# Performance work log

Measured on AMD Instinct MI355X. Metric: run time of the kernel, lower is better.

Reference implementation:

```python
import jax, jax.numpy as jnp
import numpy as np

C_IN = 128
C_INNER = 128


def setup_inputs() -> dict:
    key = jax.random.key(0)
    ks = jax.random.split(key, 9)
    b, c, h, w = 4, C_IN, 64, 64
    s = 1.0 / np.sqrt(c)
    x = jax.random.normal(ks[0], (b, c, h, w), dtype=jnp.float32)
    Wq = jax.random.normal(ks[1], (C_INNER, C_IN), dtype=jnp.float32) * s
    bq = jnp.zeros((C_INNER,), dtype=jnp.float32)
    Wk = jax.random.normal(ks[2], (C_INNER, C_IN), dtype=jnp.float32) * s
    bk = jnp.zeros((C_INNER,), dtype=jnp.float32)
    Wv = jax.random.normal(ks[3], (C_INNER, C_IN), dtype=jnp.float32) * s
    bv = jnp.zeros((C_INNER,), dtype=jnp.float32)
    Wo = jax.random.normal(ks[4], (C_IN, C_INNER), dtype=jnp.float32) * (1.0 / np.sqrt(C_INNER))
    bo = jnp.zeros((C_IN,), dtype=jnp.float32)
    return {"x": x, "Wq": Wq, "bq": bq, "Wk": Wk, "bk": bk,
            "Wv": Wv, "bv": bv, "Wo": Wo, "bo": bo}


def _conv1x1(x, W, bias):
    # x: (b,c,h,w), W: (o,c) -> (b,o,h,w)
    return jnp.einsum('oc,bchw->bohw', W, x) + bias[None, :, None, None]


def reference(x, Wq, bq, Wk, bk, Wv, bv, Wo, bo):
    b, c, h, w = x.shape
    ci = Wq.shape[0]
    n = h * w
    q = _conv1x1(x, Wq, bq).reshape(b, ci, n)          # (b, ci, n)
    k = _conv1x1(x, Wk, bk).reshape(b, ci, n)          # (b, ci, n)
    v = _conv1x1(x, Wv, bv).reshape(b, ci, n)          # (b, ci, n)
    # attn = softmax(q^T @ k) over keys
    attn = jnp.einsum('bci,bcj->bij', q, k)            # (b, n, n)
    attn = jax.nn.softmax(attn, axis=-1)
    out = jnp.einsum('bij,bcj->bci', attn, v)          # (b, ci, n)
    out = out.reshape(b, ci, h, w)
    out = _conv1x1(out, Wo, bo)
    return out + x
```

## Files before the change

### kernel.cpp

```cpp
#include <hip/hip_runtime.h>
#include <math.h>
#include <stdint.h>

#define CDIM 128
#define NTOT 4096

typedef _Float16 f16x8 __attribute__((ext_vector_type(8)));
typedef float floatx4 __attribute__((ext_vector_type(4)));

static __device__ __forceinline__ floatx4 mfma16(f16x8 a, f16x8 b, floatx4 c) {
    return __builtin_amdgcn_mfma_f32_16x16x32_f16(a, b, c, 0, 0, 0);
}
static __device__ __forceinline__ unsigned short f2h(float f) {
    _Float16 h = (_Float16)f;
    return __builtin_bit_cast(unsigned short, h);
}
static __device__ __forceinline__ float h2f(unsigned short u) {
    return (float)__builtin_bit_cast(_Float16, u);
}

#define SWZ(row, cc) ((((row) << 7)) + ((((cc) ^ ((row) & 15))) << 3))
#define SWZ8(row, cc) ((((row) << 6)) + ((((cc) ^ ((row) & 7))) << 3))

static __device__ __forceinline__ void gload_lds16(const void* g, void* l) {
    __builtin_amdgcn_global_load_lds(
        (const __attribute__((address_space(1))) void*)g,
        (__attribute__((address_space(3))) void*)l, 16, 0, 0);
}

__global__ __launch_bounds__(256) void qkv_proj_kernel(
    const float* __restrict__ x,
    const float* __restrict__ Wq, const float* __restrict__ bq,
    const float* __restrict__ Wk, const float* __restrict__ bk,
    const float* __restrict__ Wv, const float* __restrict__ bv,
    unsigned short* __restrict__ qo, unsigned short* __restrict__ ko,
    unsigned short* __restrict__ vo)
{
    __shared__ __align__(16) unsigned short Xs[64][136];
    __shared__ __align__(16) unsigned short Ws[64][136];

    const int t = threadIdx.x, b = blockIdx.y, n0 = blockIdx.x * 64;
    const int zo = blockIdx.z * 64;
    const int w = t >> 6, quad = (t >> 4) & 3, l15 = t & 15;

    {
        const int n = (t & 15) * 4;
        const int c = (t >> 4) * 8;
        float4 xr[8];
        #pragma unroll
        for (int j = 0; j < 8; ++j)
            xr[j] = *(const float4*)&x[((size_t)b * CDIM + c + j) * NTOT + n0 + n];
        #pragma unroll
        for (int k = 0; k < 4; ++k) {
            ushort4 ulo, uhi;
            ulo.x = f2h(((const float*)&xr[0])[k]);
            ulo.y = f2h(((const float*)&xr[1])[k]);
            ulo.z = f2h(((const float*)&xr[2])[k]);
            ulo.w = f2h(((const float*)&xr[3])[k]);
            uhi.x = f2h(((const float*)&xr[4])[k]);
            uhi.y = f2h(((const float*)&xr[5])[k]);
            uhi.z = f2h(((const float*)&xr[6])[k]);
            uhi.w = f2h(((const float*)&xr[7])[k]);
            *(ushort4*)&Xs[n + k][c]     = ulo;
            *(ushort4*)&Xs[n + k][c + 4] = uhi;
        }
    }

    f16x8 xf[4];
    for (int s = 0; s < 3; ++s) {
        const float* W    = (s == 0) ? Wq : (s == 1) ? Wk : Wv;
        const float* bias = (s == 0) ? bq : (s == 1) ? bk : bv;
        if (s) __syncthreads();
        {
            int o = t >> 2, ch = (t & 3) * 32;
            #pragma unroll
            for (int i = 0; i < 8; ++i) {
                float4 f4 = *(const float4*)&W[(size_t)(zo + o) * CDIM + ch + i * 4];
                ushort4 u = { f2h(f4.x), f2h(f4.y), f2h(f4.z), f2h(f4.w) };
                *(ushort4*)&Ws[o][ch + i * 4] = u;
            }
        }
        __syncthreads();
        if (s == 0) {
            #pragma unroll
            for (int f = 0; f < 4; ++f)
                xf[f] = *(const f16x8*)&Xs[w * 16 + l15][f * 32 + quad * 8];
        }

        if (s < 2) {
            unsigned short* dst = (s == 0) ? qo : ko;
            #pragma unroll
            for (int ot = 0; ot < 4; ++ot) {
                floatx4 acc = (floatx4){0.f, 0.f, 0.f, 0.f};
                #pragma unroll
                for (int f = 0; f < 4; ++f) {
                    f16x8 aW = *(const f16x8*)&Ws[ot * 16 + l15][f * 32 + quad * 8];
                    acc = mfma16(aW, xf[f], acc);
                }
                const int ob = zo + ot * 16 + quad * 4;
                ushort4 u;
                u.x = f2h(acc[0] + bias[ob + 0]);
                u.y = f2h(acc[1] + bias[ob + 1]);
                u.z = f2h(acc[2] + bias[ob + 2]);
                u.w = f2h(acc[3] + bias[ob + 3]);
                *(ushort4*)&dst[((size_t)b * NTOT + n0 + w * 16 + l15) * CDIM + ob] = u;
            }
        } else {
            #pragma unroll
            for (int ot = 0; ot < 4; ++ot) {
                floatx4 acc = (floatx4){0.f, 0.f, 0.f, 0.f};
                #pragma unroll
                for (int f = 0; f < 4; ++f) {
                    f16x8 bW = *(const f16x8*)&Ws[ot * 16 + l15][f * 32 + quad * 8];
                    acc = mfma16(xf[f], bW, acc);
                }
                const int o = zo + ot * 16 + l15;
                const float bv_ = bias[o];
                ushort4 u;
                u.x = f2h(acc[0] + bv_); u.y = f2h(acc[1] + bv_);
                u.z = f2h(acc[2] + bv_); u.w = f2h(acc[3] + bv_);
                *(ushort4*)&vo[((size_t)b * CDIM + o) * NTOT + n0 + w * 16 + quad * 4] = u;
            }
        }
    }
}

__global__ __launch_bounds__(256, 2) void attn_kernel(
    const unsigned short* __restrict__ qg,
    const unsigned short* __restrict__ kg,
    const unsigned short* __restrict__ vg,
    unsigned short* __restrict__ Op,
    float* __restrict__ Ms, float* __restrict__ Ls)
{
    __shared__ __align__(16) unsigned short Kb[2][64 * 128];
    __shared__ __align__(16) unsigned short Vb[2][128 * 64];

    const int t = threadIdx.x;
    const int w = t >> 6, quad = (t >> 4) & 3, l15 = t & 15;

    const int bid = blockIdx.x;
    const int swz = ((bid & 7) << 6) | (bid >> 3);
    const int gidx = swz >> 5;
    const int b = gidx & 3;
    const int z = gidx >> 2;
    const int i0 = (swz & 31) * 128;
    const int jbase = z * 1024;
    const size_t vbase = (size_t)b * CDIM * NTOT;

    f16x8 bQ[2][4];
    #pragma unroll
    for (int nt = 0; nt < 2; ++nt) {
        const size_t qrow = ((size_t)b * NTOT + i0 + w * 32 + nt * 16 + l15) * CDIM;
        #pragma unroll
        for (int f = 0; f < 4; ++f)
            bQ[nt][f] = *(const f16x8*)&qg[qrow + f * 32 + quad * 8];
    }

    auto stage = [&](unsigned short* Kd, unsigned short* Vd, int j0) {
        const size_t kbase = ((size_t)b * NTOT + j0) * CDIM;
        const size_t vrow0 = vbase + j0;
        #pragma unroll
        for (int r = 0; r < 4; ++r) {
            const int flat = r * 256 + t;
            const int ldsoff = (r * 256 + (t & ~63)) * 8;
            const int krow = flat >> 4, kcc = flat & 15;
            gload_lds16(&kg[kbase + (size_t)krow * CDIM + ((kcc ^ (krow & 15)) << 3)],
                        &Kd[ldsoff]);
            const int vrow = flat >> 3, vcc = flat & 7;
            gload_lds16(&vg[vrow0 + (size_t)vrow * NTOT + ((vcc ^ (vrow & 7)) << 3)],
                        &Vd[ldsoff]);
        }
    };

    floatx4 accO[2][8];
    #pragma unroll
    for (int nt = 0; nt < 2; ++nt)
        #pragma unroll
        for (int dt = 0; dt < 8; ++dt) accO[nt][dt] = (floatx4){0.f, 0.f, 0.f, 0.f};
    float m_run[2] = {-INFINITY, -INFINITY};
    float l_part[2] = {0.f, 0.f};

    stage(Kb[0], Vb[0], jbase);

    for (int iter = 0; iter < 16; ++iter) {
        const int cur = iter & 1;

        asm volatile("s_waitcnt vmcnt(0) lgkmcnt(0)" ::: "memory");
        __builtin_amdgcn_s_barrier();

        if (iter < 15) stage(Kb[cur ^ 1], Vb[cur ^ 1], jbase + (iter + 1) * 64);

        floatx4 accT[2][4];
        #pragma unroll
        for (int nt = 0; nt < 2; ++nt)
            #pragma unroll
            for (int jt = 0; jt < 4; ++jt) accT[nt][jt] = (floatx4){0.f, 0.f, 0.f, 0.f};
        #pragma unroll
        for (int jt = 0; jt < 4; ++jt)
            #pragma unroll
            for (int f = 0; f < 4; ++f) {
                f16x8 aK = *(const f16x8*)&Kb[cur][SWZ(jt * 16 + l15, f * 4 + quad)];
                accT[0][jt] = mfma16(aK, bQ[0][f], accT[0][jt]);
                accT[1][jt] = mfma16(aK, bQ[1][f], accT[1][jt]);
            }

        float m_new[2], alpha[2];
        ushort4 pu[2][4];
        #pragma unroll
        for (int nt = 0; nt < 2; ++nt) {
            float tm = accT[nt][0][0];
            #pragma unroll
            for (int jt = 0; jt < 4; ++jt)
                #pragma unroll
                for (int r = 0; r < 4; ++r) tm = fmaxf(tm, accT[nt][jt][r]);
            tm = fmaxf(tm, __shfl_xor(tm, 16));
            tm = fmaxf(tm, __shfl_xor(tm, 32));
            m_new[nt] = fmaxf(m_run[nt], tm);
            alpha[nt] = __expf(m_run[nt] - m_new[nt]);
            m_run[nt] = m_new[nt];
            float ps = 0.f;
            #pragma unroll
            for (int jt = 0; jt < 4; ++jt) {
                float p0 = __expf(accT[nt][jt][0] - m_new[nt]);
                float p1 = __expf(accT[nt][jt][1] - m_new[nt]);
                float p2 = __expf(accT[nt][jt][2] - m_new[nt]);
                float p3 = __expf(accT[nt][jt][3] - m_new[nt]);
                ps += (p0 + p1) + (p2 + p3);
                pu[nt][jt].x = f2h(p0); pu[nt][jt].y = f2h(p1);
                pu[nt][jt].z = f2h(p2); pu[nt][jt].w = f2h(p3);
            }
            l_part[nt] = l_part[nt] * alpha[nt] + ps;
            #pragma unroll
            for (int dt = 0; dt < 8; ++dt) {
                accO[nt][dt][0] *= alpha[nt]; accO[nt][dt][1] *= alpha[nt];
                accO[nt][dt][2] *= alpha[nt]; accO[nt][dt][3] *= alpha[nt];
            }
        }

        asm volatile("s_waitcnt lgkmcnt(0)" ::: "memory");
        __builtin_amdgcn_s_barrier();

        unsigned short* Pb = Kb[cur];
        #pragma unroll
        for (int nt = 0; nt < 2; ++nt) {
            const int prow = w * 32 + nt * 16 + l15;
            #pragma unroll
            for (int jt = 0; jt < 4; ++jt)
                *(ushort4*)&Pb[SWZ8(prow, 2 * jt + (quad >> 1)) + (quad & 1) * 4] =
                    pu[nt][jt];
        }

        f16x8 bP[2][2];
        #pragma unroll
        for (int nt = 0; nt < 2; ++nt) {
            const int prow = w * 32 + nt * 16 + l15;
            #pragma unroll
            for (int kb = 0; kb < 2; ++kb)
                bP[nt][kb] = *(const f16x8*)&Pb[SWZ8(prow, kb * 4 + quad)];
        }
        #pragma unroll
        for (int dt = 0; dt < 8; ++dt)
            #pragma unroll
            for (int kb = 0; kb < 2; ++kb) {
                f16x8 aV = *(const f16x8*)&Vb[cur][SWZ8(dt * 16 + l15, kb * 4 + quad)];
                accO[0][dt] = mfma16(aV, bP[0][kb], accO[0][dt]);
                accO[1][dt] = mfma16(aV, bP[1][kb], accO[1][dt]);
            }
    }

    #pragma unroll
    for (int nt = 0; nt < 2; ++nt) {
        float lf = l_part[nt];
        lf += __shfl_xor(lf, 16);
        lf += __shfl_xor(lf, 32);
        const float inv = 1.0f / lf;
        const size_t orow =
            (((size_t)z * 4 + b) * NTOT + i0 + w * 32 + nt * 16 + l15) * CDIM;
        #pragma unroll
        for (int dt = 0; dt < 8; ++dt) {
            ushort4 u;
            u.x = f2h(accO[nt][dt][0] * inv); u.y = f2h(accO[nt][dt][1] * inv);
            u.z = f2h(accO[nt][dt][2] * inv); u.w = f2h(accO[nt][dt][3] * inv);
            *(ushort4*)&Op[orow + dt * 16 + quad * 4] = u;
        }
        if (quad == 0) {
            const int idx = (z * 4 + b) * NTOT + i0 + w * 32 + nt * 16 + l15;
            Ms[idx] = m_run[nt];
            Ls[idx] = lf;
        }
    }
}

__global__ __launch_bounds__(256) void out_proj_kernel(
    const unsigned short* __restrict__ Op,
    const float* __restrict__ Ms, const float* __restrict__ Ls,
    const float* __restrict__ Wo, const float* __restrict__ bo,
    const float* __restrict__ x, float* __restrict__ out)
{
    __shared__ __align__(16) unsigned short As[64][136];
    __shared__ __align__(16) unsigned short Ws[64][136];

    const int t = threadIdx.x, b = blockIdx.y, n0 = blockIdx.x * 64;
    const int zo = blockIdx.z * 64;
    const int w = t >> 6, quad = (t >> 4) & 3, l15 = t & 15;

    const size_t PER = (size_t)NTOT * 4 * CDIM;

    #pragma unroll
    for (int r = 0; r < 4; ++r) {
        int flat = r * 256 + t;
        int row = flat >> 4, c16 = (flat & 15) * 8;
        const int bn = b * NTOT + n0 + row;
        float m0 = Ms[bn], m1 = Ms[bn + 16384], m2 = Ms[bn + 32768], m3 = Ms[bn + 49152];
        float M = fmaxf(fmaxf(m0, m1), fmaxf(m2, m3));
        float w0 = Ls[bn]         * __expf(m0 - M);
        float w1 = Ls[bn + 16384] * __expf(m1 - M);
        float w2 = Ls[bn + 32768] * __expf(m2 - M);
        float w3 = Ls[bn + 49152] * __expf(m3 - M);
        const float inv = 1.0f / (w0 + w1 + w2 + w3);
        w0 *= inv; w1 *= inv; w2 *= inv; w3 *= inv;

        const size_t base = (size_t)bn * CDIM + c16;
        uint4 a0 = *(const uint4*)&Op[base];
        uint4 a1 = *(const uint4*)&Op[PER + base];
        uint4 a2 = *(const uint4*)&Op[2 * PER + base];
        uint4 a3 = *(const uint4*)&Op[3 * PER + base];
        const unsigned short* p0 = (const unsigned short*)&a0;
        const unsigned short* p1 = (const unsigned short*)&a1;
        const unsigned short* p2 = (const unsigned short*)&a2;
        const unsigned short* p3 = (const unsigned short*)&a3;
        unsigned short mv[8];
        #pragma unroll
        for (int j = 0; j < 8; ++j)
            mv[j] = f2h(w0 * h2f(p0[j]) + w1 * h2f(p1[j]) +
                        w2 * h2f(p2[j]) + w3 * h2f(p3[j]));
        *(uint4*)&As[row][c16] = *(const uint4*)mv;
    }
    {
        int o = t >> 2, ch = (t & 3) * 32;
        #pragma unroll
        for (int i = 0; i < 8; ++i) {
            float4 f4 = *(const float4*)&Wo[(size_t)(zo + o) * CDIM + ch + i * 4];
            ushort4 u = { f2h(f4.x), f2h(f4.y), f2h(f4.z), f2h(f4.w) };
            *(ushort4*)&Ws[o][ch + i * 4] = u;
        }
    }
    __syncthreads();

    f16x8 bA[4];
    #pragma unroll
    for (int f = 0; f < 4; ++f)
        bA[f] = *(const f16x8*)&As[w * 16 + l15][f * 32 + quad * 8];

    #pragma unroll
    for (int ot = 0; ot < 4; ++ot) {
        floatx4 acc = (floatx4){0.f, 0.f, 0.f, 0.f};
        #pragma unroll
        for (int f = 0; f < 4; ++f) {
            f16x8 aW = *(const f16x8*)&Ws[ot * 16 + l15][f * 32 + quad * 8];
            acc = mfma16(aW, bA[f], acc);
        }
        const int ob = zo + ot * 16 + quad * 4;
        #pragma unroll
        for (int r = 0; r < 4; ++r) {
            size_t idx = ((size_t)b * CDIM + ob + r) * NTOT + n0 + w * 16 + l15;
            out[idx] = acc[r] + bo[ob + r] + x[idx];
        }
    }
}

extern "C" void kernel_launch(void* const* d_in, const int* in_sizes, int n_in,
                              void* d_out, int out_size, void* d_ws, size_t ws_size,
                              hipStream_t stream)
{
    const float* x  = (const float*)d_in[0];
    const float* Wq = (const float*)d_in[1];
    const float* bq = (const float*)d_in[2];
    const float* Wk = (const float*)d_in[3];
    const float* bk = (const float*)d_in[4];
    const float* Wv = (const float*)d_in[5];
    const float* bv = (const float*)d_in[6];
    const float* Wo = (const float*)d_in[7];
    const float* bo = (const float*)d_in[8];
    float* out = (float*)d_out;

    const size_t PER = (size_t)4 * CDIM * NTOT;
    unsigned short* q_ws  = (unsigned short*)d_ws;
    unsigned short* k_ws  = q_ws + PER;
    unsigned short* v_ws  = k_ws + PER;
    unsigned short* op_ws = v_ws + PER;
    float*          ms_ws = (float*)(op_ws + 4 * PER);
    float*          ls_ws = ms_ws + 4 * 16384;

    qkv_proj_kernel<<<dim3(64, 4, 2), dim3(256), 0, stream>>>(
        x, Wq, bq, Wk, bk, Wv, bv, q_ws, k_ws, v_ws);
    attn_kernel<<<dim3(512, 1, 1), dim3(256), 0, stream>>>(
        q_ws, k_ws, v_ws, op_ws, ms_ws, ls_ws);
    out_proj_kernel<<<dim3(64, 4, 2), dim3(256), 0, stream>>>(
        op_ws, ms_ws, ls_ws, Wo, bo, x, out);
}
```

Baseline: 144.3 us.

## Pre-convert weights to fp16, single-buffer V, lazy softmax rescale, raise occupancy

Adds a small kernel that converts all four weight matrices to fp16 once. The projection kernels then read weights directly from global memory instead of converting them into LDS per block, which drops an LDS buffer and several barriers. In the attention kernel, V becomes single-buffered and is loaded within the iteration that uses it, with a partial vmcnt wait, so LDS shrinks and launch bounds can target three blocks per SM. Online-softmax rescaling is skipped unless the running max rises by more than 8, which saves exp and multiply work. The risks are exposed V load latency, an extra kernel launch, and a small fp16 overflow risk from the stale max.

```diff
diff --git a/kernel.cpp b/kernel.cpp
--- a/kernel.cpp
+++ b/kernel.cpp
@@ -28,16 +28,27 @@
         (__attribute__((address_space(3))) void*)l, 16, 0, 0);
 }
 
+__global__ __launch_bounds__(256) void wcvt_kernel(
+    const float* __restrict__ Wq, const float* __restrict__ Wk,
+    const float* __restrict__ Wv, const float* __restrict__ Wo,
+    unsigned short* __restrict__ Wh)
+{
+    const float* src = (blockIdx.y == 0) ? Wq : (blockIdx.y == 1) ? Wk
+                     : (blockIdx.y == 2) ? Wv : Wo;
+    const int i = (blockIdx.x * 256 + threadIdx.x) * 4;
+    float4 f = *(const float4*)&src[i];
+    ushort4 u = { f2h(f.x), f2h(f.y), f2h(f.z), f2h(f.w) };
+    *(ushort4*)&Wh[(size_t)blockIdx.y * 16384 + i] = u;
+}
+
 __global__ __launch_bounds__(256) void qkv_proj_kernel(
-    const float* __restrict__ x,
-    const float* __restrict__ Wq, const float* __restrict__ bq,
-    const float* __restrict__ Wk, const float* __restrict__ bk,
-    const float* __restrict__ Wv, const float* __restrict__ bv,
+    const float* __restrict__ x, const unsigned short* __restrict__ Wh,
+    const float* __restrict__ bq, const float* __restrict__ bk,
+    const float* __restrict__ bv,
     unsigned short* __restrict__ qo, unsigned short* __restrict__ ko,
     unsigned short* __restrict__ vo)
 {
     __shared__ __align__(16) unsigned short Xs[64][136];
-    __shared__ __align__(16) unsigned short Ws[64][136];
 
     const int t = threadIdx.x, b = blockIdx.y, n0 = blockIdx.x * 64;
     const int zo = blockIdx.z * 64;
@@ -65,67 +76,58 @@
             *(ushort4*)&Xs[n + k][c + 4] = uhi;
         }
     }
+    __syncthreads();
 
     f16x8 xf[4];
-    for (int s = 0; s < 3; ++s) {
-        const float* W    = (s == 0) ? Wq : (s == 1) ? Wk : Wv;
-        const float* bias = (s == 0) ? bq : (s == 1) ? bk : bv;
-        if (s) __syncthreads();
-        {
-            int o = t >> 2, ch = (t & 3) * 32;
-            #pragma unroll
-            for (int i = 0; i < 8; ++i) {
-                float4 f4 = *(const float4*)&W[(size_t)(zo + o) * CDIM + ch + i * 4];
-                ushort4 u = { f2h(f4.x), f2h(f4.y), f2h(f4.z), f2h(f4.w) };
-                *(ushort4*)&Ws[o][ch + i * 4] = u;
-            }
-        }
-        __syncthreads();
-        if (s == 0) {
-            #pragma unroll
-            for (int f = 0; f < 4; ++f)
-                xf[f] = *(const f16x8*)&Xs[w * 16 + l15][f * 32 + quad * 8];
-        }
-
-        if (s < 2) {
-            unsigned short* dst = (s == 0) ? qo : ko;
-            #pragma unroll
-            for (int ot = 0; ot < 4; ++ot) {
-                floatx4 acc = (floatx4){0.f, 0.f, 0.f, 0.f};
-                #pragma unroll
-                for (int f = 0; f < 4; ++f) {
-                    f16x8 aW = *(const f16x8*)&Ws[ot * 16 + l15][f * 32 + quad * 8];
-                    acc = mfma16(aW, xf[f], acc);
-                }
-                const int ob = zo + ot * 16 + quad * 4;
-                ushort4 u;
-                u.x = f2h(acc[0] + bias[ob + 0]);
-                u.y = f2h(acc[1] + bias[ob + 1]);
-                u.z = f2h(acc[2] + bias[ob + 2]);
-                u.w = f2h(acc[3] + bias[ob + 3]);
-                *(ushort4*)&dst[((size_t)b * NTOT + n0 + w * 16 + l15) * CDIM + ob] = u;
-            }
-        } else {
-            #pragma unroll
-            for (int ot = 0; ot < 4; ++ot) {
-                floatx4 acc = (floatx4){0.f, 0.f, 0.f, 0.f};
-                #pragma unroll
-                for (int f = 0; f < 4; ++f) {
-                    f16x8 bW = *(const f16x8*)&Ws[ot * 16 + l15][f * 32 + quad * 8];
-                    acc = mfma16(xf[f], bW, acc);
-                }
-                const int o = zo + ot * 16 + l15;
-                const float bv_ = bias[o];
-                ushort4 u;
-                u.x = f2h(acc[0] + bv_); u.y = f2h(acc[1] + bv_);
-                u.z = f2h(acc[2] + bv_); u.w = f2h(acc[3] + bv_);
-                *(ushort4*)&vo[((size_t)b * CDIM + o) * NTOT + n0 + w * 16 + quad * 4] = u;
-            }
-        }
-    }
-}
-
-__global__ __launch_bounds__(256, 2) void attn_kernel(
+    #pragma unroll
+    for (int f = 0; f < 4; ++f)
+        xf[f] = *(const f16x8*)&Xs[w * 16 + l15][f * 32 + quad * 8];
+
+    #pragma unroll
+    for (int s = 0; s < 2; ++s) {
+        const unsigned short* Wm = Wh + (size_t)s * 16384;
+        const float* bias = s ? bk : bq;
+        unsigned short* dst = s ? ko : qo;
+        #pragma unroll
+        for (int ot = 0; ot < 4; ++ot) {
+            floatx4 acc = (floatx4){0.f, 0.f, 0.f, 0.f};
+            #pragma unroll
+            for (int f = 0; f < 4; ++f) {
+                f16x8 aW = *(const f16x8*)
+                    &Wm[(size_t)(zo + ot * 16 + l15) * CDIM + f * 32 + quad * 8];
+                acc = mfma16(aW, xf[f], acc);
+            }
+            const int ob = zo + ot * 16 + quad * 4;
+            ushort4 u;
+            u.x = f2h(acc[0] + bias[ob + 0]);
+            u.y = f2h(acc[1] + bias[ob + 1]);
+            u.z = f2h(acc[2] + bias[ob + 2]);
+            u.w = f2h(acc[3] + bias[ob + 3]);
+            *(ushort4*)&dst[((size_t)b * NTOT + n0 + w * 16 + l15) * CDIM + ob] = u;
+        }
+    }
+    {
+        const unsigned short* Wm = Wh + 2 * 16384;
+        #pragma unroll
+        for (int ot = 0; ot < 4; ++ot) {
+            floatx4 acc = (floatx4){0.f, 0.f, 0.f, 0.f};
+            #pragma unroll
+            for (int f = 0; f < 4; ++f) {
+                f16x8 bW = *(const f16x8*)
+                    &Wm[(size_t)(zo + ot * 16 + l15) * CDIM + f * 32 + quad * 8];
+                acc = mfma16(xf[f], bW, acc);
+            }
+            const int o = zo + ot * 16 + l15;
+            const float bv_ = bv[o];
+            ushort4 u;
+            u.x = f2h(acc[0] + bv_); u.y = f2h(acc[1] + bv_);
+            u.z = f2h(acc[2] + bv_); u.w = f2h(acc[3] + bv_);
+            *(ushort4*)&vo[((size_t)b * CDIM + o) * NTOT + n0 + w * 16 + quad * 4] = u;
+        }
+    }
+}
+
+__global__ __launch_bounds__(256, 3) void attn_kernel(
     const unsigned short* __restrict__ qg,
     const unsigned short* __restrict__ kg,
     const unsigned short* __restrict__ vg,
@@ -133,7 +135,7 @@
     float* __restrict__ Ms, float* __restrict__ Ls)
 {
     __shared__ __align__(16) unsigned short Kb[2][64 * 128];
-    __shared__ __align__(16) unsigned short Vb[2][128 * 64];
+    __shared__ __align__(16) unsigned short Vs[128 * 64];
 
     const int t = threadIdx.x;
     const int w = t >> 6, quad = (t >> 4) & 3, l15 = t & 15;
@@ -156,9 +158,8 @@
             bQ[nt][f] = *(const f16x8*)&qg[qrow + f * 32 + quad * 8];
     }
 
-    auto stage = [&](unsigned short* Kd, unsigned short* Vd, int j0) {
+    auto stageK = [&](unsigned short* Kd, int j0) {
         const size_t kbase = ((size_t)b * NTOT + j0) * CDIM;
-        const size_t vrow0 = vbase + j0;
         #pragma unroll
         for (int r = 0; r < 4; ++r) {
             const int flat = r * 256 + t;
@@ -166,9 +167,17 @@
             const int krow = flat >> 4, kcc = flat & 15;
             gload_lds16(&kg[kbase + (size_t)krow * CDIM + ((kcc ^ (krow & 15)) << 3)],
                         &Kd[ldsoff]);
+        }
+    };
+    auto stageV = [&](int j0) {
+        const size_t vrow0 = vbase + j0;
+        #pragma unroll
+        for (int r = 0; r < 4; ++r) {
+            const int flat = r * 256 + t;
+            const int ldsoff = (r * 256 + (t & ~63)) * 8;
             const int vrow = flat >> 3, vcc = flat & 7;
             gload_lds16(&vg[vrow0 + (size_t)vrow * NTOT + ((vcc ^ (vrow & 7)) << 3)],
-                        &Vd[ldsoff]);
+                        &Vs[ldsoff]);
         }
     };
 
@@ -180,15 +189,17 @@
     float m_run[2] = {-INFINITY, -INFINITY};
     float l_part[2] = {0.f, 0.f};
 
-    stage(Kb[0], Vb[0], jbase);
+    stageK(Kb[0], jbase);
 
     for (int iter = 0; iter < 16; ++iter) {
         const int cur = iter & 1;
+        const int j0 = jbase + iter * 64;
 
         asm volatile("s_waitcnt vmcnt(0) lgkmcnt(0)" ::: "memory");
         __builtin_amdgcn_s_barrier();
 
-        if (iter < 15) stage(Kb[cur ^ 1], Vb[cur ^ 1], jbase + (iter + 1) * 64);
+        stageV(j0);
+        if (iter < 15) stageK(Kb[cur ^ 1], j0 + 64);
 
         floatx4 accT[2][4];
         #pragma unroll
@@ -204,7 +215,6 @@
                 accT[1][jt] = mfma16(aK, bQ[1][f], accT[1][jt]);
             }
 
-        float m_new[2], alpha[2];
         ushort4 pu[2][4];
         #pragma unroll
         for (int nt = 0; nt < 2; ++nt) {
@@ -215,29 +225,36 @@
                 for (int r = 0; r < 4; ++r) tm = fmaxf(tm, accT[nt][jt][r]);
             tm = fmaxf(tm, __shfl_xor(tm, 16));
             tm = fmaxf(tm, __shfl_xor(tm, 32));
-            m_new[nt] = fmaxf(m_run[nt], tm);
-            alpha[nt] = __expf(m_run[nt] - m_new[nt]);
-            m_run[nt] = m_new[nt];
+            if (__ballot(tm > m_run[nt] + 8.f)) {
+                const float m_new = fmaxf(m_run[nt], tm);
+                const float alpha = __expf(m_run[nt] - m_new);
+                m_run[nt] = m_new;
+                l_part[nt] *= alpha;
+                #pragma unroll
+                for (int dt = 0; dt < 8; ++dt) {
+                    accO[nt][dt][0] *= alpha; accO[nt][dt][1] *= alpha;
+                    accO[nt][dt][2] *= alpha; accO[nt][dt][3] *= alpha;
+                }
+            }
+            const float mcur = m_run[nt];
             float ps = 0.f;
             #pragma unroll
             for (int jt = 0; jt < 4; ++jt) {
-                float p0 = __expf(accT[nt][jt][0] - m_new[nt]);
-                float p1 = __expf(accT[nt][jt][1] - m_new[nt]);
-                float p2 = __expf(accT[nt][jt][2] - m_new[nt]);
-                float p3 = __expf(accT[nt][jt][3] - m_new[nt]);
+                float p0 = __expf(accT[nt][jt][0] - mcur);
+                float p1 = __expf(accT[nt][jt][1] - mcur);
+                float p2 = __expf(accT[nt][jt][2] - mcur);
+                float p3 = __expf(accT[nt][jt][3] - mcur);
                 ps += (p0 + p1) + (p2 + p3);
                 pu[nt][jt].x = f2h(p0); pu[nt][jt].y = f2h(p1);
                 pu[nt][jt].z = f2h(p2); pu[nt][jt].w = f2h(p3);
             }
-            l_part[nt] = l_part[nt] * alpha[nt] + ps;
-            #pragma unroll
-            for (int dt = 0; dt < 8; ++dt) {
-                accO[nt][dt][0] *= alpha[nt]; accO[nt][dt][1] *= alpha[nt];
-                accO[nt][dt][2] *= alpha[nt]; accO[nt][dt][3] *= alpha[nt];
-            }
-        }
-
-        asm volatile("s_waitcnt lgkmcnt(0)" ::: "memory");
+            l_part[nt] += ps;
+        }
+
+        if (iter < 15)
+            asm volatile("s_waitcnt lgkmcnt(0) vmcnt(4)" ::: "memory");
+        else
+            asm volatile("s_waitcnt lgkmcnt(0) vmcnt(0)" ::: "memory");
         __builtin_amdgcn_s_barrier();
 
         unsigned short* Pb = Kb[cur];
@@ -262,7 +279,7 @@
         for (int dt = 0; dt < 8; ++dt)
             #pragma unroll
             for (int kb = 0; kb < 2; ++kb) {
-                f16x8 aV = *(const f16x8*)&Vb[cur][SWZ8(dt * 16 + l15, kb * 4 + quad)];
+                f16x8 aV = *(const f16x8*)&Vs[SWZ8(dt * 16 + l15, kb * 4 + quad)];
                 accO[0][dt] = mfma16(aV, bP[0][kb], accO[0][dt]);
                 accO[1][dt] = mfma16(aV, bP[1][kb], accO[1][dt]);
             }
@@ -294,11 +311,10 @@
 __global__ __launch_bounds__(256) void out_proj_kernel(
     const unsigned short* __restrict__ Op,
     const float* __restrict__ Ms, const float* __restrict__ Ls,
-    const float* __restrict__ Wo, const float* __restrict__ bo,
+    const unsigned short* __restrict__ Woh, const float* __restrict__ bo,
     const float* __restrict__ x, float* __restrict__ out)
 {
     __shared__ __align__(16) unsigned short As[64][136];
-    __shared__ __align__(16) unsigned short Ws[64][136];
 
     const int t = threadIdx.x, b = blockIdx.y, n0 = blockIdx.x * 64;
     const int zo = blockIdx.z * 64;
@@ -336,15 +352,6 @@
                         w2 * h2f(p2[j]) + w3 * h2f(p3[j]));
         *(uint4*)&As[row][c16] = *(const uint4*)mv;
     }
-    {
-        int o = t >> 2, ch = (t & 3) * 32;
-        #pragma unroll
-        for (int i = 0; i < 8; ++i) {
-            float4 f4 = *(const float4*)&Wo[(size_t)(zo + o) * CDIM + ch + i * 4];
-            ushort4 u = { f2h(f4.x), f2h(f4.y), f2h(f4.z), f2h(f4.w) };
-            *(ushort4*)&Ws[o][ch + i * 4] = u;
-        }
-    }
     __syncthreads();
 
     f16x8 bA[4];
@@ -357,7 +364,8 @@
         floatx4 acc = (floatx4){0.f, 0.f, 0.f, 0.f};
         #pragma unroll
         for (int f = 0; f < 4; ++f) {
-            f16x8 aW = *(const f16x8*)&Ws[ot * 16 + l15][f * 32 + quad * 8];
+            f16x8 aW = *(const f16x8*)
+                &Woh[(size_t)(zo + ot * 16 + l15) * CDIM + f * 32 + quad * 8];
             acc = mfma16(aW, bA[f], acc);
         }
         const int ob = zo + ot * 16 + quad * 4;
@@ -391,11 +399,13 @@
     unsigned short* op_ws = v_ws + PER;
     float*          ms_ws = (float*)(op_ws + 4 * PER);
     float*          ls_ws = ms_ws + 4 * 16384;
-
+    unsigned short* wh_ws = (unsigned short*)(ls_ws + 4 * 16384);
+
+    wcvt_kernel<<<dim3(16, 4), dim3(256), 0, stream>>>(Wq, Wk, Wv, Wo, wh_ws);
     qkv_proj_kernel<<<dim3(64, 4, 2), dim3(256), 0, stream>>>(
-        x, Wq, bq, Wk, bk, Wv, bv, q_ws, k_ws, v_ws);
+        x, wh_ws, bq, bk, bv, q_ws, k_ws, v_ws);
     attn_kernel<<<dim3(512, 1, 1), dim3(256), 0, stream>>>(
         q_ws, k_ws, v_ws, op_ws, ms_ws, ls_ws);
     out_proj_kernel<<<dim3(64, 4, 2), dim3(256), 0, stream>>>(
-        op_ws, ms_ws, ls_ws, Wo, bo, x, out);
-}
+        op_ws, ms_ws, ls_ws, wh_ws + 3 * 16384, bo, x, out);
+}
```

Result: slower. 161.4 us (+11.8%).
